# Performance work log

Hardware: AMD Instinct MI355X
Metric: run time of the kernel (lower is better)

## Reference

```python
import jax, jax.numpy as jnp
from jax import lax
import numpy as np

D_IN, D, H, W, POOL = 1280, 100, 20, 3, 9
K_SIG, X0 = 1.0, 0.0
EPS = 1e-5


def setup_inputs() -> dict:
    key = jax.random.key(0)
    ks = jax.random.split(key, 8)
    N1, N2 = 512, 512
    return {
        "x1": jax.random.normal(ks[0], (N1, D_IN), jnp.float32),
        "x2": jax.random.normal(ks[1], (N2, D_IN), jnp.float32),
        "W1": jax.random.normal(ks[2], (D, D_IN), jnp.float32) * 0.02,
        "b1": jnp.zeros((D,), jnp.float32),
        "W2": jax.random.normal(ks[3], (H, 2 * D), jnp.float32) * 0.05,
        "b2": jnp.zeros((H,), jnp.float32),
        "bn1_g": jnp.ones((H,), jnp.float32),
        "bn1_b": jnp.zeros((H,), jnp.float32),
        "conv_w": jax.random.normal(ks[4], (1, H, 2 * W + 1, 2 * W + 1), jnp.float32) * 0.05,
        "conv_b": jnp.zeros((1,), jnp.float32),
        "bn2_g": jnp.ones((1,), jnp.float32),
        "bn2_b": jnp.zeros((1,), jnp.float32),
        "gamma": jnp.zeros((1,), jnp.float32),
    }


def reference(x1, x2, W1, b1, W2, b2, bn1_g, bn1_b, conv_w, conv_b, bn2_g, bn2_b, gamma):
    N1, N2 = x1.shape[0], x2.shape[0]
    # fc1 projection (relu1/dropout1 are defined but unused in the original forward)
    a = (x1 @ W1.T + b1)[None]          # [1, N1, D]
    c = (x2 @ W1.T + b2 * 0 + b1)[None] if False else (x2 @ W1.T + b1)[None]  # [1, N2, D]
    # broadcast pairwise |diff| and product -> [1, N1, N2, 2D]
    diff = jnp.abs(a[:, :, None, :] - c[:, None, :, :])
    mul = a[:, :, None, :] * c[:, None, :, :]
    m = jnp.concatenate([diff, mul], axis=-1).reshape(-1, 2 * D)  # [N1*N2, 2D]
    # fc2
    m = m @ W2.T + b2                    # [N1*N2, H]
    # BatchNorm1d in training mode: batch statistics, biased variance
    mu = m.mean(axis=0)
    var = m.var(axis=0)
    m = (m - mu) * lax.rsqrt(var + EPS) * bn1_g + bn1_b
    m = jax.nn.relu(m)
    m = m.reshape(1, N1, N2, H).transpose(0, 3, 1, 2)  # NCHW [1, H, N1, N2]
    # 7x7 conv, padding=W
    C = lax.conv_general_dilated(m, conv_w, (1, 1), [(W, W), (W, W)])
    C = C + conv_b.reshape(1, -1, 1, 1)
    # BatchNorm2d (training mode, biased variance over N,H,W per channel)
    mu2 = C.mean(axis=(0, 2, 3), keepdims=True)
    var2 = C.var(axis=(0, 2, 3), keepdims=True)
    C = (C - mu2) * lax.rsqrt(var2 + EPS) * bn2_g.reshape(1, -1, 1, 1) + bn2_b.reshape(1, -1, 1, 1)
    C = jax.nn.sigmoid(C)
    # MaxPool2d(9, padding=4): stride = kernel, -inf padding
    p = POOL // 2
    B = lax.reduce_window(C, -jnp.inf, lax.max, (1, 1, POOL, POOL), (1, 1, POOL, POOL),
                          [(0, 0), (0, 0), (p, p), (p, p)])
    # mean / unbiased std over dims (1, 2) keepdim
    mean = B.mean(axis=(1, 2), keepdims=True)
    std = jnp.sqrt(B.var(axis=(1, 2), keepdims=True, ddof=1) + EPS)
    Q = jax.nn.relu(B - mean - gamma.reshape(()) * std)
    phat = Q.sum() / (jnp.sign(Q).sum() + 1.0)
    phat = jnp.clip(jax.nn.sigmoid(K_SIG * (phat - X0)), 0.0, 1.0)
    return phat, C
```

## Files before the change

### kernel.cpp

```cpp
#include <hip/hip_runtime.h>
#include <hip/hip_bf16.h>
#include <math.h>

#define N1 512
#define N2 512
#define DIN 1280
#define DD 100
#define HH 20
#define NPIX (N1*N2)
#define PB 57
#define NWIN (PB*PB)

typedef short bf16x8 __attribute__((ext_vector_type(8)));
typedef float f32x4 __attribute__((ext_vector_type(4)));

static __device__ __forceinline__ float bf16f(unsigned short u) {
  union { unsigned int i; float f; } c;
  c.i = ((unsigned int)u) << 16;
  return c.f;
}

static constexpr size_t WS_PP    = 0;
static constexpr size_t WS_W1T   = 409600;
static constexpr size_t WS_W2B   = 537600;
static constexpr size_t WS_M     = 541696;
static constexpr size_t WS_PART  = WS_M + 2621440;
static constexpr size_t WS_CRAW  = WS_PART + 1310720;
static constexpr size_t WS_STATS = WS_CRAW + 262144;
static constexpr size_t WS_B     = WS_STATS + 64;

__global__ __launch_bounds__(256) void kP(const float* __restrict__ W1,
                                          float* __restrict__ w1t) {
  const int tid = threadIdx.x;
  __shared__ float sT[32][33];
  const int bx = blockIdx.x % 40, by = blockIdx.x / 40;
  const int tx = tid & 31, ty = tid >> 5;
#pragma unroll
  for (int e = 0; e < 4; ++e) {
    int h = by * 32 + ty + e * 8, k = bx * 32 + tx;
    sT[ty + e * 8][tx] = (h < DD) ? W1[(size_t)h * DIN + k] : 0.0f;
  }
  __syncthreads();
#pragma unroll
  for (int e = 0; e < 4; ++e) {
    int k = bx * 32 + ty + e * 8, h = by * 32 + tx;
    if (h < DD) w1t[(size_t)k * DD + h] = sT[tx][ty + e * 8];
  }
}

__global__ __launch_bounds__(256) void kA(const float* __restrict__ x1,
                                          const float* __restrict__ x2,
                                          const float* __restrict__ w1t,
                                          const float* __restrict__ W2,
                                          float* __restrict__ pp,
                                          unsigned short* __restrict__ w2b,
                                          float* __restrict__ stats) {
  const int tid = threadIdx.x;
  if (blockIdx.x >= 1024) {
    int idx = (blockIdx.x - 1024) * 256 + tid;
    if (blockIdx.x == 1024 && tid < 64) stats[tid] = 0.0f;
    if (idx < 224 * 32) {
      int k = idx >> 5, n = idx & 31;
      float v = (n < HH && k < 200) ? W2[n * 200 + k] : 0.0f;
      __hip_bfloat16 b = __float2bfloat16(v);
      w2b[idx] = *reinterpret_cast<unsigned short*>(&b);
    }
    return;
  }
  const int w  = __builtin_amdgcn_readfirstlane(tid >> 6);
  const int rp = w >> 1, hh = w & 1;
  const int h = hh * 64 + (tid & 63);
  if (h >= DD) return;
  const int kq = blockIdx.x & 3;
  const int r0 = (blockIdx.x >> 2) * 4 + rp * 2;
  const float* xb = (r0 < N1) ? (x1 + (size_t)r0 * DIN) : (x2 + (size_t)(r0 - N1) * DIN);
  const float* xr0 = xb + kq * 320;
  const float* xr1 = xb + DIN + kq * 320;
  const float* w1p = w1t + (size_t)kq * 320 * DD + h;
  float a00 = 0.f, a01 = 0.f, a10 = 0.f, a11 = 0.f;
#pragma unroll 8
  for (int k = 0; k < 320; k += 2) {
    float wA = w1p[(size_t)k * DD];
    float wB = w1p[(size_t)(k + 1) * DD];
    a00 = fmaf(wA, xr0[k], a00); a01 = fmaf(wB, xr0[k + 1], a01);
    a10 = fmaf(wA, xr1[k], a10); a11 = fmaf(wB, xr1[k + 1], a11);
  }
  pp[(size_t)kq * 102400 + (size_t)r0 * DD + h] = a00 + a01;
  pp[(size_t)kq * 102400 + (size_t)(r0 + 1) * DD + h] = a10 + a11;
}

__global__ __launch_bounds__(256, 2) void kB(const float* __restrict__ pp,
                                             const float* __restrict__ b1,
                                             const unsigned short* __restrict__ w2b,
                                             unsigned short* __restrict__ m16,
                                             float* __restrict__ stats) {
  __shared__ float sA[8][132];
  __shared__ float sC[64][132];
  __shared__ float wred[4][40];
  const int tid = threadIdx.x;
  const int band = blockIdx.x & 7;
  const int bi = band * 8 + ((blockIdx.x >> 3) & 7);
  const int bj = blockIdx.x >> 6;
  for (int idx = tid; idx < 72 * 33; idx += 256) {
    int r = idx / 33, d4 = idx % 33;
    float4 v = {0.f, 0.f, 0.f, 0.f};
    if (d4 < 25) {
      size_t row = (r < 8) ? (size_t)(bi * 8 + r) : (size_t)(N1 + bj * 64 + (r - 8));
      const float* base = pp + row * DD;
      float4 a0 = ((const float4*)base)[d4];
      float4 a1 = ((const float4*)(base + 102400))[d4];
      float4 a2 = ((const float4*)(base + 204800))[d4];
      float4 a3 = ((const float4*)(base + 307200))[d4];
      float4 bb = ((const float4*)b1)[d4];
      v.x = a0.x + a1.x + a2.x + a3.x + bb.x;
      v.y = a0.y + a1.y + a2.y + a3.y + bb.y;
      v.z = a0.z + a1.z + a2.z + a3.z + bb.z;
      v.w = a0.w + a1.w + a2.w + a3.w + bb.w;
    }
    if (r < 8) *(float4*)&sA[r][4 * d4] = v;
    else       *(float4*)&sC[r - 8][4 * d4] = v;
  }
  __syncthreads();
  const int w = tid >> 6, lane = tid & 63;
  const int ln = lane & 15, q = lane >> 4;
  const int jj = w * 16 + ln;
  bf16x8 af[7][2];
#pragma unroll
  for (int ks = 0; ks < 7; ++ks)
#pragma unroll
    for (int t = 0; t < 2; ++t) {
      bf16x8 v;
#pragma unroll
      for (int e = 0; e < 8; ++e)
        v[e] = (short)w2b[(ks * 32 + q * 8 + e) * 32 + ln + 16 * t];
      af[ks][t] = v;
    }
  int dOf[14];
  bool isP[14];
  float4 cH[14];
#pragma unroll
  for (int hx = 0; hx < 14; ++hx) {
    int kk = (hx >> 1) * 32 + q * 8 + (hx & 1) * 4;
    isP[hx] = kk >= 100;
    dOf[hx] = isP[hx] ? kk - 100 : kk;
    cH[hx] = *(const float4*)&sC[jj][dOf[hx]];
  }
  float st_s[8], st_q[8];
#pragma unroll
  for (int r = 0; r < 8; ++r) { st_s[r] = 0.f; st_q[r] = 0.f; }
  const int gj = bj * 64 + jj;
#pragma unroll 1
  for (int ii = 0; ii < 8; ++ii) {
    bf16x8 bf[7];
#pragma unroll
    for (int ks = 0; ks < 7; ++ks) {
      float4 a0 = *(const float4*)&sA[ii][dOf[2 * ks]];
      float4 a1 = *(const float4*)&sA[ii][dOf[2 * ks + 1]];
      float4 c0 = cH[2 * ks], c1 = cH[2 * ks + 1];
      float f0 = isP[2*ks]   ? a0.x * c0.x : fabsf(a0.x - c0.x);
      float f1 = isP[2*ks]   ? a0.y * c0.y : fabsf(a0.y - c0.y);
      float f2 = isP[2*ks]   ? a0.z * c0.z : fabsf(a0.z - c0.z);
      float f3 = isP[2*ks]   ? a0.w * c0.w : fabsf(a0.w - c0.w);
      float f4 = isP[2*ks+1] ? a1.x * c1.x : fabsf(a1.x - c1.x);
      float f5 = isP[2*ks+1] ? a1.y * c1.y : fabsf(a1.y - c1.y);
      float f6 = isP[2*ks+1] ? a1.z * c1.z : fabsf(a1.z - c1.z);
      float f7 = isP[2*ks+1] ? a1.w * c1.w : fabsf(a1.w - c1.w);
      union { bf16x8 v; __hip_bfloat162 h2[4]; } u;
      u.h2[0] = __float22bfloat162_rn(make_float2(f0, f1));
      u.h2[1] = __float22bfloat162_rn(make_float2(f2, f3));
      u.h2[2] = __float22bfloat162_rn(make_float2(f4, f5));
      u.h2[3] = __float22bfloat162_rn(make_float2(f6, f7));
      bf[ks] = u.v;
    }
    f32x4 acc0 = {0.f, 0.f, 0.f, 0.f}, acc1 = {0.f, 0.f, 0.f, 0.f};
#pragma unroll
    for (int ks = 0; ks < 7; ++ks) {
      acc0 = __builtin_amdgcn_mfma_f32_16x16x32_bf16(af[ks][0], bf[ks], acc0, 0, 0, 0);
      acc1 = __builtin_amdgcn_mfma_f32_16x16x32_bf16(af[ks][1], bf[ks], acc1, 0, 0, 0);
    }
    const size_t pix = (size_t)(bi * 8 + ii) * N2 + gj;
#pragma unroll
    for (int r = 0; r < 4; ++r) {
      __hip_bfloat16 hb = __float2bfloat16(acc0[r]);
      m16[(size_t)(4 * q + r) * NPIX + pix] = *reinterpret_cast<unsigned short*>(&hb);
      st_s[r] += acc0[r];
      st_q[r] += acc0[r] * acc0[r];
    }
    if (q == 0) {
#pragma unroll
      for (int r = 0; r < 4; ++r) {
        __hip_bfloat16 hb = __float2bfloat16(acc1[r]);
        m16[(size_t)(16 + r) * NPIX + pix] = *reinterpret_cast<unsigned short*>(&hb);
      }
    }
#pragma unroll
    for (int r = 0; r < 4; ++r) {
      st_s[4 + r] += acc1[r];
      st_q[4 + r] += acc1[r] * acc1[r];
    }
  }
#pragma unroll
  for (int r = 0; r < 8; ++r) {
#pragma unroll
    for (int off = 1; off < 16; off <<= 1) {
      st_s[r] += __shfl_xor(st_s[r], off);
      st_q[r] += __shfl_xor(st_q[r], off);
    }
  }
  if (ln == 0) {
#pragma unroll
    for (int r = 0; r < 4; ++r) {
      wred[w][4 * q + r]      = st_s[r];
      wred[w][20 + 4 * q + r] = st_q[r];
    }
    if (q == 0) {
#pragma unroll
      for (int r = 0; r < 4; ++r) {
        wred[w][16 + r] = st_s[4 + r];
        wred[w][36 + r] = st_q[4 + r];
      }
    }
  }
  __syncthreads();
  if (tid < 40)
    atomicAdd(&stats[tid], wred[0][tid] + wred[1][tid] + wred[2][tid] + wred[3][tid]);
}

__global__ __launch_bounds__(256) void kD(const unsigned short* __restrict__ m16,
                                          const float* __restrict__ bn1g,
                                          const float* __restrict__ bn1b,
                                          const float* __restrict__ cw,
                                          const float* __restrict__ stats,
                                          float* __restrict__ part) {
  __shared__ float sIn[4][22][74];
  __shared__ float sSc[4], sSh[4];
  const int tid = threadIdx.x;
  const int band = blockIdx.x & 7;
  const int rest = blockIdx.x >> 3;
  const int cs   = rest >> 5;
  const int t    = rest & 31;
  const int by   = (band * 4 + (t & 3)) * 16;
  const int bx   = (t >> 2) * 64;
  if (tid < 4) {
    int ch = cs * 4 + tid;
    float s = stats[ch], q = stats[HH + ch];
    float mu = s * (1.0f / NPIX);
    float var = q * (1.0f / NPIX) - mu * mu;
    float g = bn1g[ch] / sqrtf(var + 1e-5f);
    sSc[tid] = g;
    sSh[tid] = bn1b[ch] - mu * g;
  }
  __syncthreads();
  for (int idx = tid; idx < 4 * 22 * 18; idx += 256) {
    int ch4 = idx / (22 * 18), rem = idx % (22 * 18);
    int r = rem / 18, p = rem % 18;
    int gy = by + r - 3;
    int gx0 = bx + 4 * p - 4;
    float sc = sSc[ch4], sh = sSh[ch4];
    float v[4] = {0.f, 0.f, 0.f, 0.f};
    if (gy >= 0 && gy < N1) {
      const unsigned short* mp = m16 + (size_t)(cs * 4 + ch4) * NPIX + (size_t)gy * N2;
      if (gx0 >= 0 && gx0 + 3 < N2) {
        ushort4 u = *(const ushort4*)&mp[gx0];
        v[0] = fmaxf(fmaf(bf16f(u.x), sc, sh), 0.0f);
        v[1] = fmaxf(fmaf(bf16f(u.y), sc, sh), 0.0f);
        v[2] = fmaxf(fmaf(bf16f(u.z), sc, sh), 0.0f);
        v[3] = fmaxf(fmaf(bf16f(u.w), sc, sh), 0.0f);
      } else {
#pragma unroll
        for (int j = 0; j < 4; ++j) {
          int gx = gx0 + j;
          if (gx >= 0 && gx < N2)
            v[j] = fmaxf(fmaf(bf16f(mp[gx]), sc, sh), 0.0f);
        }
      }
    }
    *(float4*)&sIn[ch4][r][4 * p] = make_float4(v[0], v[1], v[2], v[3]);
  }
  __syncthreads();
  const int tx = tid & 31, ty = tid >> 5;
  float acc00 = 0.f, acc01 = 0.f, acc10 = 0.f, acc11 = 0.f;
#pragma unroll 1
  for (int ch4 = 0; ch4 < 4; ++ch4) {
    const float* wch = cw + (cs * 4 + ch4) * 49;
#pragma unroll
    for (int wr = 0; wr < 8; ++wr) {
      float2 rowv[5];
#pragma unroll
      for (int qq = 0; qq < 5; ++qq)
        rowv[qq] = *(const float2*)&sIn[ch4][2 * ty + wr][2 * tx + 2 * qq];
#pragma unroll
      for (int o = 0; o < 2; ++o) {
        if (wr - o < 0 || wr - o > 6) continue;
        const int ky = wr - o;
#pragma unroll
        for (int kx = 0; kx < 7; ++kx) {
          float wt = wch[ky * 7 + kx];
          const int j0 = kx + 1, j1 = kx + 2;
          float e0 = (j0 & 1) ? rowv[j0 >> 1].y : rowv[j0 >> 1].x;
          float e1 = (j1 & 1) ? rowv[j1 >> 1].y : rowv[j1 >> 1].x;
          if (o == 0) { acc00 = fmaf(e0, wt, acc00); acc01 = fmaf(e1, wt, acc01); }
          else        { acc10 = fmaf(e0, wt, acc10); acc11 = fmaf(e1, wt, acc11); }
        }
      }
    }
  }
  float* dst = part + (size_t)cs * NPIX;
  const int ox = bx + 2 * tx;
  float2 r0 = {acc00, acc01}, r1 = {acc10, acc11};
  *(float2*)&dst[(size_t)(by + 2 * ty) * N2 + ox] = r0;
  *(float2*)&dst[(size_t)(by + 2 * ty + 1) * N2 + ox] = r1;
}

__global__ __launch_bounds__(256) void kE1(const float* __restrict__ part,
                                           float* __restrict__ stats,
                                           float* __restrict__ Craw) {
  __shared__ float wred[4][2];
  const int band = blockIdx.x & 7;
  const int sub  = blockIdx.x >> 3;
  const int i = ((band << 7) + sub) * 256 + threadIdx.x;
  float s5 = part[i] + part[NPIX + i] + part[2 * NPIX + i] + part[3 * NPIX + i] + part[4 * NPIX + i];
  Craw[i] = s5;
  float s = s5, q = s5 * s5;
  const int lane = threadIdx.x & 63, wv = threadIdx.x >> 6;
#pragma unroll
  for (int off = 32; off; off >>= 1) {
    s += __shfl_xor(s, off);
    q += __shfl_xor(q, off);
  }
  if (lane == 0) { wred[wv][0] = s; wred[wv][1] = q; }
  __syncthreads();
  if (threadIdx.x < 2) {
    float v = wred[0][threadIdx.x] + wred[1][threadIdx.x] + wred[2][threadIdx.x] + wred[3][threadIdx.x];
    atomicAdd(&stats[2 * HH + threadIdx.x], v);
  }
}

__global__ __launch_bounds__(256) void kE2M(const float* __restrict__ Craw,
                                            const float* __restrict__ stats,
                                            const float* __restrict__ bn2g,
                                            const float* __restrict__ bn2b,
                                            float* __restrict__ Cout,
                                            float* __restrict__ B) {
  const int w = blockIdx.x * 4 + (threadIdx.x >> 6);
  const int lane = threadIdx.x & 63;
  float s = stats[2 * HH], q = stats[2 * HH + 1];
  float mu = s * (1.0f / NPIX);
  float var = q * (1.0f / NPIX) - mu * mu;
  float g = bn2g[0] / sqrtf(var + 1e-5f);
  float b = bn2b[0] - mu * g;
  if (w >= NWIN) return;
  const int wy = w / PB, wx = w % PB;
  const int y0 = wy * 9 - 4, x0 = wx * 9 - 4;
  float mx = -1e30f;
  for (int e = lane; e < 144; e += 64) {
    int dy = e / 12, dx = e % 12;
    int y = y0 + dy, x = x0 + dx;
    bool inWin = (dy < 9) && (dx < 9);
    bool claim = (y >= 0) && (y < N1) && (x >= 0) && (x < N2) &&
                 (dy < 9 || wy == PB - 1) && (dx < 9 || wx == PB - 1);
    if (claim) {
      float z = Craw[(size_t)y * N2 + x] * g + b;
      float sg = 1.0f / (1.0f + expf(-z));
      Cout[(size_t)y * N2 + x] = sg;
      if (inWin) mx = fmaxf(mx, sg);
    }
  }
#pragma unroll
  for (int off = 32; off; off >>= 1) mx = fmaxf(mx, __shfl_xor(mx, off));
  if (lane == 0) B[w] = mx;
}

__global__ __launch_bounds__(1024) void kF(const float* __restrict__ B,
                                           const float* __restrict__ gamma,
                                           float* __restrict__ out0) {
  __shared__ float sB[NWIN];
  __shared__ float cm[PB], cs[PB];
  __shared__ float r1[16], r2[16];
  const int tid = threadIdx.x;
  for (int i = tid; i < NWIN; i += 1024) sB[i] = B[i];
  __syncthreads();
  if (tid < PB * 16) {
    int c = tid >> 4, g = tid & 15;
    float s = 0.0f;
    for (int h = g; h < PB; h += 16) s += sB[h * PB + c];
#pragma unroll
    for (int off = 1; off < 16; off <<= 1) s += __shfl_xor(s, off);
    float mean = s / (float)PB;
    float v = 0.0f;
    for (int h = g; h < PB; h += 16) { float d = sB[h * PB + c] - mean; v += d * d; }
#pragma unroll
    for (int off = 1; off < 16; off <<= 1) v += __shfl_xor(v, off);
    if (g == 0) {
      cm[c] = mean;
      cs[c] = sqrtf(v / (float)(PB - 1) + 1e-5f);
    }
  }
  __syncthreads();
  const float g = gamma[0];
  float sq = 0.0f, cnt = 0.0f;
  for (int i = tid; i < NWIN; i += 1024) {
    int w = i % PB;
    float qv = sB[i] - cm[w] - g * cs[w];
    if (qv > 0.0f) { sq += qv; cnt += 1.0f; }
  }
#pragma unroll
  for (int off = 32; off; off >>= 1) {
    sq += __shfl_xor(sq, off);
    cnt += __shfl_xor(cnt, off);
  }
  if ((tid & 63) == 0) { r1[tid >> 6] = sq; r2[tid >> 6] = cnt; }
  __syncthreads();
  if (tid == 0) {
    float S = 0.f, Cn = 0.f;
#pragma unroll
    for (int e = 0; e < 16; ++e) { S += r1[e]; Cn += r2[e]; }
    float phat = S / (Cn + 1.0f);
    float sig = 1.0f / (1.0f + expf(-phat));
    out0[0] = fminf(fmaxf(sig, 0.0f), 1.0f);
  }
}

extern "C" void kernel_launch(void* const* d_in, const int* in_sizes, int n_in,
                              void* d_out, int out_size, void* d_ws, size_t ws_size,
                              hipStream_t stream) {
  const float* x1    = (const float*)d_in[0];
  const float* x2    = (const float*)d_in[1];
  const float* W1    = (const float*)d_in[2];
  const float* b1    = (const float*)d_in[3];
  const float* W2    = (const float*)d_in[4];
  const float* bn1g  = (const float*)d_in[6];
  const float* bn1b  = (const float*)d_in[7];
  const float* convw = (const float*)d_in[8];
  const float* bn2g  = (const float*)d_in[10];
  const float* bn2b  = (const float*)d_in[11];
  const float* gamma = (const float*)d_in[12];

  float* ws    = (float*)d_ws;
  float* pp    = ws + WS_PP;
  float* w1t   = ws + WS_W1T;
  unsigned short* w2b = (unsigned short*)(ws + WS_W2B);
  unsigned short* m16 = (unsigned short*)(ws + WS_M);
  float* part  = ws + WS_PART;
  float* Craw  = ws + WS_CRAW;
  float* stats = ws + WS_STATS;
  float* Bp    = ws + WS_B;
  float* out   = (float*)d_out;

  kP<<<160, 256, 0, stream>>>(W1, w1t);
  kA<<<1052, 256, 0, stream>>>(x1, x2, w1t, W2, pp, w2b, stats);
  kB<<<512, 256, 0, stream>>>(pp, b1, w2b, m16, stats);
  kD<<<1280, 256, 0, stream>>>(m16, bn1g, bn1b, convw, stats, part);
  kE1<<<1024, 256, 0, stream>>>(part, stats, Craw);
  kE2M<<<(NWIN + 3) / 4, 256, 0, stream>>>(Craw, stats, bn2g, bn2b, out + 1, Bp);
  kF<<<1, 1024, 0, stream>>>(Bp, gamma, out);
}
```

Before: 88.37 us.

## Drop W1 transpose kernel, read W1 rows directly, and split kB rows across twice the blocks

```diff
diff --git a/kernel.cpp b/kernel.cpp
--- a/kernel.cpp
+++ b/kernel.cpp
@@ -21,36 +21,16 @@
 }
 
 static constexpr size_t WS_PP    = 0;
-static constexpr size_t WS_W1T   = 409600;
-static constexpr size_t WS_W2B   = 537600;
-static constexpr size_t WS_M     = 541696;
+static constexpr size_t WS_W2B   = 409600;
+static constexpr size_t WS_M     = 413696;
 static constexpr size_t WS_PART  = WS_M + 2621440;
 static constexpr size_t WS_CRAW  = WS_PART + 1310720;
 static constexpr size_t WS_STATS = WS_CRAW + 262144;
 static constexpr size_t WS_B     = WS_STATS + 64;
 
-__global__ __launch_bounds__(256) void kP(const float* __restrict__ W1,
-                                          float* __restrict__ w1t) {
-  const int tid = threadIdx.x;
-  __shared__ float sT[32][33];
-  const int bx = blockIdx.x % 40, by = blockIdx.x / 40;
-  const int tx = tid & 31, ty = tid >> 5;
-#pragma unroll
-  for (int e = 0; e < 4; ++e) {
-    int h = by * 32 + ty + e * 8, k = bx * 32 + tx;
-    sT[ty + e * 8][tx] = (h < DD) ? W1[(size_t)h * DIN + k] : 0.0f;
-  }
-  __syncthreads();
-#pragma unroll
-  for (int e = 0; e < 4; ++e) {
-    int k = bx * 32 + ty + e * 8, h = by * 32 + tx;
-    if (h < DD) w1t[(size_t)k * DD + h] = sT[tx][ty + e * 8];
-  }
-}
-
 __global__ __launch_bounds__(256) void kA(const float* __restrict__ x1,
                                           const float* __restrict__ x2,
-                                          const float* __restrict__ w1t,
+                                          const float* __restrict__ W1,
                                           const float* __restrict__ W2,
                                           float* __restrict__ pp,
                                           unsigned short* __restrict__ w2b,
@@ -76,14 +56,19 @@
   const float* xb = (r0 < N1) ? (x1 + (size_t)r0 * DIN) : (x2 + (size_t)(r0 - N1) * DIN);
   const float* xr0 = xb + kq * 320;
   const float* xr1 = xb + DIN + kq * 320;
-  const float* w1p = w1t + (size_t)kq * 320 * DD + h;
+  const float4* wr = (const float4*)(W1 + (size_t)h * DIN + kq * 320);
   float a00 = 0.f, a01 = 0.f, a10 = 0.f, a11 = 0.f;
-#pragma unroll 8
-  for (int k = 0; k < 320; k += 2) {
-    float wA = w1p[(size_t)k * DD];
-    float wB = w1p[(size_t)(k + 1) * DD];
-    a00 = fmaf(wA, xr0[k], a00); a01 = fmaf(wB, xr0[k + 1], a01);
-    a10 = fmaf(wA, xr1[k], a10); a11 = fmaf(wB, xr1[k + 1], a11);
+#pragma unroll 4
+  for (int k4 = 0; k4 < 80; ++k4) {
+    float4 wv = wr[k4];
+    float x00 = xr0[4 * k4], x01 = xr0[4 * k4 + 1];
+    float x02 = xr0[4 * k4 + 2], x03 = xr0[4 * k4 + 3];
+    float x10 = xr1[4 * k4], x11 = xr1[4 * k4 + 1];
+    float x12 = xr1[4 * k4 + 2], x13 = xr1[4 * k4 + 3];
+    a00 = fmaf(wv.x, x00, a00); a01 = fmaf(wv.y, x01, a01);
+    a00 = fmaf(wv.z, x02, a00); a01 = fmaf(wv.w, x03, a01);
+    a10 = fmaf(wv.x, x10, a10); a11 = fmaf(wv.y, x11, a11);
+    a10 = fmaf(wv.z, x12, a10); a11 = fmaf(wv.w, x13, a11);
   }
   pp[(size_t)kq * 102400 + (size_t)r0 * DD + h] = a00 + a01;
   pp[(size_t)kq * 102400 + (size_t)(r0 + 1) * DD + h] = a10 + a11;
@@ -94,18 +79,21 @@
                                              const unsigned short* __restrict__ w2b,
                                              unsigned short* __restrict__ m16,
                                              float* __restrict__ stats) {
-  __shared__ float sA[8][132];
+  __shared__ float sA[4][132];
   __shared__ float sC[64][132];
   __shared__ float wred[4][40];
   const int tid = threadIdx.x;
-  const int band = blockIdx.x & 7;
-  const int bi = band * 8 + ((blockIdx.x >> 3) & 7);
-  const int bj = blockIdx.x >> 6;
-  for (int idx = tid; idx < 72 * 33; idx += 256) {
+  const int half = blockIdx.x & 1;
+  const int rest = blockIdx.x >> 1;
+  const int band = rest & 7;
+  const int bi = band * 8 + ((rest >> 3) & 7);
+  const int bj = rest >> 6;
+  const int rowBase = bi * 8 + half * 4;
+  for (int idx = tid; idx < 68 * 33; idx += 256) {
     int r = idx / 33, d4 = idx % 33;
     float4 v = {0.f, 0.f, 0.f, 0.f};
     if (d4 < 25) {
-      size_t row = (r < 8) ? (size_t)(bi * 8 + r) : (size_t)(N1 + bj * 64 + (r - 8));
+      size_t row = (r < 4) ? (size_t)(rowBase + r) : (size_t)(N1 + bj * 64 + (r - 4));
       const float* base = pp + row * DD;
       float4 a0 = ((const float4*)base)[d4];
       float4 a1 = ((const float4*)(base + 102400))[d4];
@@ -117,8 +105,8 @@
       v.z = a0.z + a1.z + a2.z + a3.z + bb.z;
       v.w = a0.w + a1.w + a2.w + a3.w + bb.w;
     }
-    if (r < 8) *(float4*)&sA[r][4 * d4] = v;
-    else       *(float4*)&sC[r - 8][4 * d4] = v;
+    if (r < 4) *(float4*)&sA[r][4 * d4] = v;
+    else       *(float4*)&sC[r - 4][4 * d4] = v;
   }
   __syncthreads();
   const int w = tid >> 6, lane = tid & 63;
@@ -150,7 +138,7 @@
   for (int r = 0; r < 8; ++r) { st_s[r] = 0.f; st_q[r] = 0.f; }
   const int gj = bj * 64 + jj;
 #pragma unroll 1
-  for (int ii = 0; ii < 8; ++ii) {
+  for (int ii = 0; ii < 4; ++ii) {
     bf16x8 bf[7];
 #pragma unroll
     for (int ks = 0; ks < 7; ++ks) {
@@ -178,7 +166,7 @@
       acc0 = __builtin_amdgcn_mfma_f32_16x16x32_bf16(af[ks][0], bf[ks], acc0, 0, 0, 0);
       acc1 = __builtin_amdgcn_mfma_f32_16x16x32_bf16(af[ks][1], bf[ks], acc1, 0, 0, 0);
     }
-    const size_t pix = (size_t)(bi * 8 + ii) * N2 + gj;
+    const size_t pix = (size_t)(rowBase + ii) * N2 + gj;
 #pragma unroll
     for (int r = 0; r < 4; ++r) {
       __hip_bfloat16 hb = __float2bfloat16(acc0[r]);
@@ -438,7 +426,6 @@
 
   float* ws    = (float*)d_ws;
   float* pp    = ws + WS_PP;
-  float* w1t   = ws + WS_W1T;
   unsigned short* w2b = (unsigned short*)(ws + WS_W2B);
   unsigned short* m16 = (unsigned short*)(ws + WS_M);
   float* part  = ws + WS_PART;
@@ -447,9 +434,8 @@
   float* Bp    = ws + WS_B;
   float* out   = (float*)d_out;
 
-  kP<<<160, 256, 0, stream>>>(W1, w1t);
-  kA<<<1052, 256, 0, stream>>>(x1, x2, w1t, W2, pp, w2b, stats);
-  kB<<<512, 256, 0, stream>>>(pp, b1, w2b, m16, stats);
+  kA<<<1052, 256, 0, stream>>>(x1, x2, W1, W2, pp, w2b, stats);
+  kB<<<1024, 256, 0, stream>>>(pp, b1, w2b, m16, stats);
   kD<<<1280, 256, 0, stream>>>(m16, bn1g, bn1b, convw, stats, part);
   kE1<<<1024, 256, 0, stream>>>(part, stats, Craw);
   kE2M<<<(NWIN + 3) / 4, 256, 0, stream>>>(Craw, stats, bn2g, bn2b, out + 1, Bp);
```

New measurement: 113.0 us. 27.8% more time.
